# Kernel tuning notes

Measured on AMD Instinct MI355X. Metric: run time of the kernel, lower is better.

Reference implementation:

```python
import jax, jax.numpy as jnp
import numpy as np

N_NODES = 100000
N_EDGES = 6400000
D_IN = 256
OUT = 2        # heads=1, out_channels=2 -> H*C = 2
NEG_SLOPE = 0.2


def setup_inputs() -> dict:
    key = jax.random.key(0)
    ks = jax.random.split(key, 10)
    x = jax.random.normal(ks[0], (N_NODES, D_IN), dtype=jnp.float32)
    edge_index = jax.random.randint(ks[1], (2, N_EDGES), 0, N_NODES, dtype=jnp.int64)
    edge_attr = jax.random.normal(ks[2], (N_EDGES, 1), dtype=jnp.float32)
    s = 1.0 / np.sqrt(D_IN)
    # GATv2Conv params: lin_l (src), lin_r (dst) with bias; lin_edge no bias; att [H*C]; out bias
    Wl = jax.random.normal(ks[3], (D_IN, OUT), dtype=jnp.float32) * s
    bl = jnp.zeros((OUT,), dtype=jnp.float32)
    Wr = jax.random.normal(ks[4], (D_IN, OUT), dtype=jnp.float32) * s
    br = jnp.zeros((OUT,), dtype=jnp.float32)
    We = jax.random.normal(ks[5], (1, OUT), dtype=jnp.float32)
    att = jax.random.normal(ks[6], (OUT,), dtype=jnp.float32)
    bias = jnp.zeros((OUT,), dtype=jnp.float32)
    return {"x": x, "edge_index": edge_index, "edge_attr": edge_attr,
            "Wl": Wl, "bl": bl, "Wr": Wr, "br": br, "We": We,
            "att": att, "bias": bias}


def reference(x, edge_index, edge_attr, Wl, bl, Wr, br, We, att, bias):
    N = x.shape[0]
    src, tgt = edge_index[0], edge_index[1]  # messages flow src -> tgt
    xl = x @ Wl + bl                          # [N, OUT] source-side transform
    xr = x @ Wr + br                          # [N, OUT] target-side transform
    # per-edge GATv2 score: leaky_relu(xl_j + xr_i + W_e e_ij) . att
    m = xl[src] + xr[tgt] + edge_attr @ We    # [E, OUT]
    m = jax.nn.leaky_relu(m, NEG_SLOPE)
    alpha = m @ att                           # [E]
    # segment softmax over edges sharing the same target node
    amax = jax.ops.segment_max(alpha, tgt, num_segments=N)
    amax = jnp.where(jnp.isfinite(amax), amax, 0.0)
    ex = jnp.exp(alpha - amax[tgt])
    denom = jax.ops.segment_sum(ex, tgt, num_segments=N)
    a = ex / (denom[tgt] + 1e-16)             # [E]
    out = jax.ops.segment_sum(a[:, None] * xl[src], tgt, num_segments=N)
    return out + bias
```

## Files before the change

kernel.cpp:

```cpp
#include <hip/hip_runtime.h>

#define N_NODES 100000
#define N_EDGES 6400000
#define D_IN 256
constexpr float NEG_SLOPE = 0.2f;

#define NR 32
#define RANGE 3125
#define NG 16

#define NCH 1280
#define CHE 5000
#define CAP 232
#define HALFCAP 116
#define CPG 80
#define PFLAT (CPG * HALFCAP)
#define NB ((PFLAT + 1023) / 1024)
#define BBLK 256
#define CBLK 1024

#define FCHE 400000


__global__ void node_transform(const float* __restrict__ x,
                               const float* __restrict__ Wl, const float* __restrict__ bl,
                               const float* __restrict__ Wr, const float* __restrict__ br,
                               float* __restrict__ xl, float* __restrict__ xr) {
    int wave = (blockIdx.x * blockDim.x + threadIdx.x) >> 6;
    int lane = threadIdx.x & 63;
    if (wave >= N_NODES) return;
    const float4 xv  = *reinterpret_cast<const float4*>(x + (size_t)wave * D_IN + lane * 4);
    const float4 wlA = *reinterpret_cast<const float4*>(Wl + lane * 8);
    const float4 wlB = *reinterpret_cast<const float4*>(Wl + lane * 8 + 4);
    const float4 wrA = *reinterpret_cast<const float4*>(Wr + lane * 8);
    const float4 wrB = *reinterpret_cast<const float4*>(Wr + lane * 8 + 4);
    float sl0 = xv.x*wlA.x + xv.y*wlA.z + xv.z*wlB.x + xv.w*wlB.z;
    float sl1 = xv.x*wlA.y + xv.y*wlA.w + xv.z*wlB.y + xv.w*wlB.w;
    float sr0 = xv.x*wrA.x + xv.y*wrA.z + xv.z*wrB.x + xv.w*wrB.z;
    float sr1 = xv.x*wrA.y + xv.y*wrA.w + xv.z*wrB.y + xv.w*wrB.w;
    #pragma unroll
    for (int o = 32; o > 0; o >>= 1) {
        sl0 += __shfl_xor(sl0, o);
        sl1 += __shfl_xor(sl1, o);
        sr0 += __shfl_xor(sr0, o);
        sr1 += __shfl_xor(sr1, o);
    }
    if (lane == 0) {
        xl[2*wave]   = sl0 + bl[0];
        xl[2*wave+1] = sl1 + bl[1];
        xr[2*wave]   = sr0 + br[0];
        xr[2*wave+1] = sr1 + br[1];
    }
}

__global__ void detect_dtype(const int* __restrict__ ei32, int* __restrict__ flag) {
    int lane = threadIdx.x;
    int v = ei32[2 * lane + 1];
    unsigned long long nz = __ballot(v != 0);
    if (lane == 0) *flag = (nz == 0ull) ? 1 : 0;
}


__device__ __forceinline__ void bucket_one(int src, int tgt, float ea,
                                           float2* __restrict__ recs,
                                           int* __restrict__ cnt, int c) {
    const int r  = tgt / RANGE;
    const int li = tgt - r * RANGE;
    const int slot = atomicAdd(&cnt[r], 1);
    if (slot < CAP) {
        float2 rec;
        rec.x = __uint_as_float((unsigned)src | ((unsigned)li << 17));
        rec.y = ea;
        recs[(size_t)(c * NR + r) * CAP + slot] = rec;
    }
}

template <bool IS64>
__device__ __forceinline__ void bucket_loop(const void* __restrict__ ei,
                                            const float* __restrict__ eattr,
                                            float2* __restrict__ recs,
                                            int* __restrict__ cnt, int c) {
    const int base = c * CHE;
    const int end  = base + CHE;
    for (int j = 0; j < CHE; j += BBLK * 4) {
        const int e0 = base + j + (int)threadIdx.x * 4;
        if (e0 + 4 <= end) {
            int4 sv, tv;
            if (IS64) {
                const int4* ps = (const int4*)((const long long*)ei + e0);
                int4 a = ps[0], b = ps[1];
                sv = make_int4(a.x, a.z, b.x, b.z);
                const int4* pt = (const int4*)((const long long*)ei + N_EDGES + e0);
                int4 cc = pt[0], dd = pt[1];
                tv = make_int4(cc.x, cc.z, dd.x, dd.z);
            } else {
                sv = *(const int4*)((const int*)ei + e0);
                tv = *(const int4*)((const int*)ei + N_EDGES + e0);
            }
            const float4 ev = *(const float4*)(eattr + e0);
            bucket_one(sv.x, tv.x, ev.x, recs, cnt, c);
            bucket_one(sv.y, tv.y, ev.y, recs, cnt, c);
            bucket_one(sv.z, tv.z, ev.z, recs, cnt, c);
            bucket_one(sv.w, tv.w, ev.w, recs, cnt, c);
        } else if (e0 < end) {
            for (int e = e0; e < end && e < e0 + 4; ++e) {
                int src, tgt;
                if (IS64) { src = (int)((const long long*)ei)[e]; tgt = (int)((const long long*)ei)[N_EDGES + e]; }
                else      { src = ((const int*)ei)[e];            tgt = ((const int*)ei)[N_EDGES + e]; }
                bucket_one(src, tgt, eattr[e], recs, cnt, c);
            }
        }
    }
}

__global__ __launch_bounds__(BBLK) void bucket_pass(const void* __restrict__ ei,
                                                    const float* __restrict__ eattr,
                                                    float2* __restrict__ recs,
                                                    int* __restrict__ counts,
                                                    const int* __restrict__ flag) {
    __shared__ int cnt[NR];
    const int c = blockIdx.x;
    if (threadIdx.x < NR) cnt[threadIdx.x] = 0;
    __syncthreads();
    if (*flag) bucket_loop<true >(ei, eattr, recs, cnt, c);
    else       bucket_loop<false>(ei, eattr, recs, cnt, c);
    __syncthreads();
    if (threadIdx.x < NR) {
        int v = cnt[threadIdx.x];
        counts[c * NR + threadIdx.x] = v < CAP ? v : CAP;
    }
}

__global__ __launch_bounds__(CBLK, 8) void gather_accum(const float2* __restrict__ recs,
                                                        const int* __restrict__ counts,
                                                        const float* __restrict__ xl,
                                                        const float* __restrict__ xr,
                                                        const float* __restrict__ We,
                                                        const float* __restrict__ att,
                                                        float* __restrict__ partial) {
    __shared__ float  acc[RANGE * 3];
    __shared__ float2 xrs[RANGE];
    __shared__ int    tag[RANGE];
    __shared__ int    s_n[CPG];
    const int r = blockIdx.x & (NR - 1);
    const int g = blockIdx.x >> 5;
    const int lo = r * RANGE;
    for (int i = threadIdx.x; i < RANGE * 3; i += CBLK) acc[i] = 0.f;
    for (int i = threadIdx.x; i < RANGE; i += CBLK) xrs[i] = ((const float2*)xr)[lo + i];
    for (int i = threadIdx.x; i < CPG; i += CBLK) s_n[i] = counts[(g * CPG + i) * NR + r];
    __syncthreads();
    const float we0 = We[0], we1 = We[1];
    const float a0 = att[0], a1 = att[1];
    const float2* xl2 = (const float2*)xl;
    const int c0 = g * CPG;
    const int tid = threadIdx.x;

    auto fetch_pair = [&](int pidx, unsigned& vm) -> float4 {
        float4 out = make_float4(0.f, 0.f, 0.f, 0.f);
        vm = 0u;
        if (pidx < PFLAT) {
            const int cc = pidx / HALFCAP;
            const int i  = pidx - cc * HALFCAP;
            const int n  = s_n[cc];
            if (2 * i < n) {
                const float2* seg = recs + (size_t)((c0 + cc) * NR + r) * CAP;
                out = ((const float4*)seg)[i];
                vm = (2 * i + 1 < n) ? 3u : 1u;
            }
        }
        return out;
    };

    unsigned vCur, vNxt, vFly;
    float4 curP = fetch_pair(tid, vCur);
    float4 nxtP = fetch_pair(CBLK + tid, vNxt);
    float2 xsA0 = make_float2(0.f, 0.f), xsA1 = make_float2(0.f, 0.f);
    if (vCur & 1u) xsA0 = xl2[__float_as_uint(curP.x) & 0x1FFFF];
    if (vCur & 2u) xsA1 = xl2[__float_as_uint(curP.z) & 0x1FFFF];

    bool d0 = false, d1 = false;
    int  dl0 = 0, dl1 = 0;
    float dc00 = 0.f, dc01 = 0.f, de0 = 0.f, dc10 = 0.f, dc11 = 0.f, de1 = 0.f;

    for (int b = 0; b < NB; ++b) {
        float4 flyP = fetch_pair((b + 2) * CBLK + tid, vFly);
        float2 xsB0 = make_float2(0.f, 0.f), xsB1 = make_float2(0.f, 0.f);
        if (vNxt & 1u) xsB0 = xl2[__float_as_uint(nxtP.x) & 0x1FFFF];
        if (vNxt & 2u) xsB1 = xl2[__float_as_uint(nxtP.z) & 0x1FFFF];

        const bool h0 = (vCur & 1u) != 0u, h1 = (vCur & 2u) != 0u;
        int li0 = 0, li1 = 0;
        float ex0 = 0.f, cv00 = 0.f, cv01 = 0.f;
        float ex1 = 0.f, cv10 = 0.f, cv11 = 0.f;
        if (h0) {
            const unsigned p = __float_as_uint(curP.x);
            li0 = p >> 17;
            const float2 xt = xrs[li0];
            float m0 = xsA0.x + xt.x + curP.y * we0;
            float m1 = xsA0.y + xt.y + curP.y * we1;
            m0 = m0 > 0.f ? m0 : NEG_SLOPE * m0;
            m1 = m1 > 0.f ? m1 : NEG_SLOPE * m1;
            ex0  = __expf(m0 * a0 + m1 * a1);
            cv00 = ex0 * xsA0.x;
            cv01 = ex0 * xsA0.y;
            tag[li0] = tid;
        }
        if (h1) {
            const unsigned p = __float_as_uint(curP.z);
            li1 = p >> 17;
            const float2 xt = xrs[li1];
            float m0 = xsA1.x + xt.x + curP.w * we0;
            float m1 = xsA1.y + xt.y + curP.w * we1;
            m0 = m0 > 0.f ? m0 : NEG_SLOPE * m0;
            m1 = m1 > 0.f ? m1 : NEG_SLOPE * m1;
            ex1  = __expf(m0 * a0 + m1 * a1);
            cv10 = ex1 * xsA1.x;
            cv11 = ex1 * xsA1.y;
            tag[li1] = tid;
        }
        if (d0) {
            float* bp = acc + dl0 * 3;
            atomicAdd(bp + 0, dc00); atomicAdd(bp + 1, dc01); atomicAdd(bp + 2, de0);
            d0 = false;
        }
        if (d1) {
            float* bp = acc + dl1 * 3;
            atomicAdd(bp + 0, dc10); atomicAdd(bp + 1, dc11); atomicAdd(bp + 2, de1);
            d1 = false;
        }
        __syncthreads();
        if (h0) {
            if (tag[li0] == tid) {
                float* bp = acc + li0 * 3;
                bp[0] += cv00; bp[1] += cv01; bp[2] += ex0;
            } else {
                d0 = true; dl0 = li0; dc00 = cv00; dc01 = cv01; de0 = ex0;
            }
        }
        if (h1) {
            if (tag[li1] == tid) {
                float* bp = acc + li1 * 3;
                bp[0] += cv10; bp[1] += cv11; bp[2] += ex1;
            } else {
                d1 = true; dl1 = li1; dc10 = cv10; dc11 = cv11; de1 = ex1;
            }
        }
        __syncthreads();
        curP = nxtP; vCur = vNxt; xsA0 = xsB0; xsA1 = xsB1;
        nxtP = flyP; vNxt = vFly;
    }
    if (d0) {
        float* bp = acc + dl0 * 3;
        atomicAdd(bp + 0, dc00); atomicAdd(bp + 1, dc01); atomicAdd(bp + 2, de0);
    }
    if (d1) {
        float* bp = acc + dl1 * 3;
        atomicAdd(bp + 0, dc10); atomicAdd(bp + 1, dc11); atomicAdd(bp + 2, de1);
    }
    __syncthreads();

    float* dst = partial + (size_t)(r * NG + g) * (RANGE * 3);
    for (int i = threadIdx.x; i < RANGE * 3; i += CBLK) dst[i] = acc[i];
}

template <bool IS64>
__device__ __forceinline__ void scan_loop(const void* __restrict__ ei,
                                          const float* __restrict__ eattr,
                                          const float2* __restrict__ xl2,
                                          const float2* __restrict__ xr2,
                                          float we0, float we1, float a0, float a1,
                                          int lo, int eBeg, int eEnd,
                                          float* __restrict__ acc) {
    for (int e = eBeg + (int)threadIdx.x; e < eEnd; e += CBLK) {
        int tgt;
        if (IS64) tgt = (int)((const long long*)ei)[N_EDGES + e];
        else      tgt = ((const int*)ei)[N_EDGES + e];
        unsigned li = (unsigned)(tgt - lo);
        if (li < RANGE) {
            int src;
            if (IS64) src = (int)((const long long*)ei)[e];
            else      src = ((const int*)ei)[e];
            const float ea = eattr[e];
            const float2 xs = xl2[src];
            const float2 xt = xr2[tgt];
            float m0 = xs.x + xt.x + ea * we0;
            float m1 = xs.y + xt.y + ea * we1;
            m0 = m0 > 0.f ? m0 : NEG_SLOPE * m0;
            m1 = m1 > 0.f ? m1 : NEG_SLOPE * m1;
            const float ex = __expf(m0 * a0 + m1 * a1);
            float* b = acc + li * 3u;
            atomicAdd(b + 0, ex * xs.x);
            atomicAdd(b + 1, ex * xs.y);
            atomicAdd(b + 2, ex);
        }
    }
}

__global__ __launch_bounds__(CBLK) void edge_scan(const void* __restrict__ ei,
                                                  const float* __restrict__ eattr,
                                                  const float* __restrict__ xl,
                                                  const float* __restrict__ xr,
                                                  const float* __restrict__ We,
                                                  const float* __restrict__ att,
                                                  float* __restrict__ partial,
                                                  const int* __restrict__ flag) {
    __shared__ float acc[RANGE * 3];
    const int r = blockIdx.x & (NR - 1);
    const int g = blockIdx.x >> 5;
    for (int i = threadIdx.x; i < RANGE * 3; i += CBLK) acc[i] = 0.f;
    __syncthreads();
    const int lo = r * RANGE;
    const int eBeg = g * FCHE, eEnd = eBeg + FCHE;
    const float we0 = We[0], we1 = We[1];
    const float a0 = att[0], a1 = att[1];
    if (*flag)
        scan_loop<true >(ei, eattr, (const float2*)xl, (const float2*)xr, we0, we1, a0, a1, lo, eBeg, eEnd, acc);
    else
        scan_loop<false>(ei, eattr, (const float2*)xl, (const float2*)xr, we0, we1, a0, a1, lo, eBeg, eEnd, acc);
    __syncthreads();
    float* dst = partial + (size_t)(r * NG + g) * (RANGE * 3);
    for (int i = threadIdx.x; i < RANGE * 3; i += CBLK) dst[i] = acc[i];
}

__global__ void reduce_partials(const float* __restrict__ partial,
                                const float* __restrict__ bias, float* __restrict__ out) {
    int i = blockIdx.x * blockDim.x + threadIdx.x;
    if (i >= N_NODES) return;
    const int r = i / RANGE;
    const int li = i - r * RANGE;
    float n0 = 0.f, n1 = 0.f, d = 0.f;
    #pragma unroll 4
    for (int g = 0; g < NG; ++g) {
        const float* p = partial + (size_t)(r * NG + g) * (RANGE * 3) + (size_t)li * 3;
        n0 += p[0]; n1 += p[1]; d += p[2];
    }
    d += 1e-16f;
    float2 o;
    o.x = n0 / d + bias[0];
    o.y = n1 / d + bias[1];
    ((float2*)out)[i] = o;
}

__global__ void edge_pass_atomic(const void* __restrict__ ei,
                                 const float* __restrict__ eattr,
                                 const float* __restrict__ xl, const float* __restrict__ xr,
                                 const float* __restrict__ We, const float* __restrict__ att,
                                 float* __restrict__ acc4, const int* __restrict__ flag) {
    const int is64 = *flag;
    const float we0 = We[0], we1 = We[1];
    const float a0 = att[0], a1 = att[1];
    const int stride = gridDim.x * blockDim.x;
    for (int e = blockIdx.x * blockDim.x + threadIdx.x; e < N_EDGES; e += stride) {
        int src, tgt;
        if (is64) { src = (int)((const long long*)ei)[e]; tgt = (int)((const long long*)ei)[N_EDGES + e]; }
        else      { src = ((const int*)ei)[e];            tgt = ((const int*)ei)[N_EDGES + e]; }
        const float ea = eattr[e];
        const float2 xs = ((const float2*)xl)[src];
        const float2 xt = ((const float2*)xr)[tgt];
        float m0 = xs.x + xt.x + ea * we0;
        float m1 = xs.y + xt.y + ea * we1;
        m0 = m0 > 0.f ? m0 : NEG_SLOPE * m0;
        m1 = m1 > 0.f ? m1 : NEG_SLOPE * m1;
        const float ex = __expf(m0 * a0 + m1 * a1);
        float* b = acc4 + (size_t)tgt * 4;
        atomicAdd(b + 0, ex * xs.x);
        atomicAdd(b + 1, ex * xs.y);
        atomicAdd(b + 2, ex);
    }
}

__global__ void finalize4(const float* __restrict__ acc4,
                          const float* __restrict__ bias, float* __restrict__ out) {
    int i = blockIdx.x * blockDim.x + threadIdx.x;
    if (i >= N_NODES) return;
    const float4 a = ((const float4*)acc4)[i];
    const float d = a.z + 1e-16f;
    float2 o;
    o.x = a.x / d + bias[0];
    o.y = a.y / d + bias[1];
    ((float2*)out)[i] = o;
}

extern "C" void kernel_launch(void* const* d_in, const int* in_sizes, int n_in,
                              void* d_out, int out_size, void* d_ws, size_t ws_size,
                              hipStream_t stream) {
    const float* x    = (const float*)d_in[0];
    const void*  ei   = d_in[1];
    const float* ea   = (const float*)d_in[2];
    const float* Wl   = (const float*)d_in[3];
    const float* bl   = (const float*)d_in[4];
    const float* Wr   = (const float*)d_in[5];
    const float* br   = (const float*)d_in[6];
    const float* We   = (const float*)d_in[7];
    const float* att  = (const float*)d_in[8];
    const float* bias = (const float*)d_in[9];

    float* ws      = (float*)d_ws;
    float* xl      = ws;
    float* xr      = ws + 2 * N_NODES;
    float* partial = ws + 4 * N_NODES;
    const size_t partial_floats = (size_t)NR * NG * RANGE * 3;
    float* recs_f  = partial + partial_floats;
    const size_t recs_floats = (size_t)NCH * NR * CAP * 2;
    int*   counts  = (int*)(recs_f + recs_floats);

    const size_t need_bucket = (4 * (size_t)N_NODES + partial_floats + recs_floats
                                + (size_t)NCH * NR + 16) * sizeof(float);
    const size_t need_scan   = (4 * (size_t)N_NODES + partial_floats + 16) * sizeof(float);

    node_transform<<<(N_NODES * 64) / 256, 256, 0, stream>>>(x, Wl, bl, Wr, br, xl, xr);

    if (ws_size >= need_bucket) {
        int* flag = counts + (size_t)NCH * NR;
        detect_dtype<<<1, 64, 0, stream>>>((const int*)ei, flag);
        bucket_pass<<<NCH, BBLK, 0, stream>>>(ei, ea, (float2*)recs_f, counts, flag);
        gather_accum<<<NR * NG, CBLK, 0, stream>>>((const float2*)recs_f, counts,
                                                   xl, xr, We, att, partial);
        reduce_partials<<<(N_NODES + 255) / 256, 256, 0, stream>>>(partial, bias, (float*)d_out);
    } else if (ws_size >= need_scan) {
        int* flag = (int*)(partial + partial_floats);
        detect_dtype<<<1, 64, 0, stream>>>((const int*)ei, flag);
        edge_scan<<<NR * NG, CBLK, 0, stream>>>(ei, ea, xl, xr, We, att, partial, flag);
        reduce_partials<<<(N_NODES + 255) / 256, 256, 0, stream>>>(partial, bias, (float*)d_out);
    } else {
        float* acc4 = ws + 4 * N_NODES;
        int* flag = (int*)(acc4 + 4 * (size_t)N_NODES);
        hipMemsetAsync(acc4, 0, (size_t)N_NODES * 4 * sizeof(float), stream);
        detect_dtype<<<1, 64, 0, stream>>>((const int*)ei, flag);
        edge_pass_atomic<<<4096, 256, 0, stream>>>(ei, ea, xl, xr, We, att, acc4, flag);
        finalize4<<<(N_NODES + 255) / 256, 256, 0, stream>>>(acc4, bias, (float*)d_out);
    }
}
```

Baseline: 124.7 us.

## Fuse node transform, dtype detect and bucketing; coarsen buckets with wave-aggregated slots

Merges the node linear transform, the index dtype detection and the edge bucketing pass into one launch, using separate block ranges for bucketing and node work. Buckets are coarsened from 32 to 16 target ranges, with larger capacity, and slot allocation uses ballot-based wave aggregation so each bucket takes one shared atomic per wave. Each gather block reads its coarse bucket and filters records down to its half range, so every record is read twice. The node transform now packs four nodes per wave. The goal is fewer launches and less shared-atomic contention, at the cost of duplicated record reads and a serial 16-way ballot loop per edge.

```diff
diff --git a/kernel.cpp b/kernel.cpp
--- a/kernel.cpp
+++ b/kernel.cpp
@@ -5,73 +5,55 @@
 #define D_IN 256
 constexpr float NEG_SLOPE = 0.2f;
 
-#define NR 32
+#define NRANGES 32
 #define RANGE 3125
 #define NG 16
 
+#define NRSEG 16
+#define SEGRANGE 6250
 #define NCH 1280
 #define CHE 5000
-#define CAP 232
-#define HALFCAP 116
+#define CAP 416
+#define HALFCAP 208
 #define CPG 80
 #define PFLAT (CPG * HALFCAP)
 #define NB ((PFLAT + 1023) / 1024)
-#define BBLK 256
+#define ABLK 256
 #define CBLK 1024
-
+#define NODE_BLKS 6250
 #define FCHE 400000
 
 
-__global__ void node_transform(const float* __restrict__ x,
-                               const float* __restrict__ Wl, const float* __restrict__ bl,
-                               const float* __restrict__ Wr, const float* __restrict__ br,
-                               float* __restrict__ xl, float* __restrict__ xr) {
-    int wave = (blockIdx.x * blockDim.x + threadIdx.x) >> 6;
-    int lane = threadIdx.x & 63;
-    if (wave >= N_NODES) return;
-    const float4 xv  = *reinterpret_cast<const float4*>(x + (size_t)wave * D_IN + lane * 4);
-    const float4 wlA = *reinterpret_cast<const float4*>(Wl + lane * 8);
-    const float4 wlB = *reinterpret_cast<const float4*>(Wl + lane * 8 + 4);
-    const float4 wrA = *reinterpret_cast<const float4*>(Wr + lane * 8);
-    const float4 wrB = *reinterpret_cast<const float4*>(Wr + lane * 8 + 4);
-    float sl0 = xv.x*wlA.x + xv.y*wlA.z + xv.z*wlB.x + xv.w*wlB.z;
-    float sl1 = xv.x*wlA.y + xv.y*wlA.w + xv.z*wlB.y + xv.w*wlB.w;
-    float sr0 = xv.x*wrA.x + xv.y*wrA.z + xv.z*wrB.x + xv.w*wrB.z;
-    float sr1 = xv.x*wrA.y + xv.y*wrA.w + xv.z*wrB.y + xv.w*wrB.w;
+__device__ __forceinline__ int alloc_slot(int r, int* __restrict__ cnt) {
+    const int lane = threadIdx.x & 63;
+    const unsigned long long lt = (1ull << lane) - 1ull;
+    int slot = 0;
     #pragma unroll
-    for (int o = 32; o > 0; o >>= 1) {
-        sl0 += __shfl_xor(sl0, o);
-        sl1 += __shfl_xor(sl1, o);
-        sr0 += __shfl_xor(sr0, o);
-        sr1 += __shfl_xor(sr1, o);
-    }
-    if (lane == 0) {
-        xl[2*wave]   = sl0 + bl[0];
-        xl[2*wave+1] = sl1 + bl[1];
-        xr[2*wave]   = sr0 + br[0];
-        xr[2*wave+1] = sr1 + br[1];
-    }
-}
-
-__global__ void detect_dtype(const int* __restrict__ ei32, int* __restrict__ flag) {
-    int lane = threadIdx.x;
-    int v = ei32[2 * lane + 1];
-    unsigned long long nz = __ballot(v != 0);
-    if (lane == 0) *flag = (nz == 0ull) ? 1 : 0;
-}
-
+    for (int rr = 0; rr < NRSEG; ++rr) {
+        const unsigned long long m = __ballot(r == rr);
+        if (r == rr) {
+            const int before = __popcll(m & lt);
+            const int leader = __ffsll((unsigned long long)m) - 1;
+            int base = 0;
+            if (lane == leader) base = atomicAdd(&cnt[rr], __popcll(m));
+            base = __shfl(base, leader);
+            slot = base + before;
+        }
+    }
+    return slot;
+}
 
 __device__ __forceinline__ void bucket_one(int src, int tgt, float ea,
                                            float2* __restrict__ recs,
                                            int* __restrict__ cnt, int c) {
-    const int r  = tgt / RANGE;
-    const int li = tgt - r * RANGE;
-    const int slot = atomicAdd(&cnt[r], 1);
+    const int r  = tgt / SEGRANGE;
+    const int li = tgt - r * SEGRANGE;
+    const int slot = alloc_slot(r, cnt);
     if (slot < CAP) {
         float2 rec;
         rec.x = __uint_as_float((unsigned)src | ((unsigned)li << 17));
         rec.y = ea;
-        recs[(size_t)(c * NR + r) * CAP + slot] = rec;
+        recs[(size_t)(c * NRSEG + r) * CAP + slot] = rec;
     }
 }
 
@@ -82,7 +64,7 @@
                                             int* __restrict__ cnt, int c) {
     const int base = c * CHE;
     const int end  = base + CHE;
-    for (int j = 0; j < CHE; j += BBLK * 4) {
+    for (int j = 0; j < CHE; j += ABLK * 4) {
         const int e0 = base + j + (int)threadIdx.x * 4;
         if (e0 + 4 <= end) {
             int4 sv, tv;
@@ -113,41 +95,93 @@
     }
 }
 
-__global__ __launch_bounds__(BBLK) void bucket_pass(const void* __restrict__ ei,
-                                                    const float* __restrict__ eattr,
-                                                    float2* __restrict__ recs,
-                                                    int* __restrict__ counts,
-                                                    const int* __restrict__ flag) {
-    __shared__ int cnt[NR];
-    const int c = blockIdx.x;
-    if (threadIdx.x < NR) cnt[threadIdx.x] = 0;
-    __syncthreads();
-    if (*flag) bucket_loop<true >(ei, eattr, recs, cnt, c);
-    else       bucket_loop<false>(ei, eattr, recs, cnt, c);
-    __syncthreads();
-    if (threadIdx.x < NR) {
-        int v = cnt[threadIdx.x];
-        counts[c * NR + threadIdx.x] = v < CAP ? v : CAP;
-    }
-}
-
-__global__ __launch_bounds__(CBLK, 8) void gather_accum(const float2* __restrict__ recs,
-                                                        const int* __restrict__ counts,
-                                                        const float* __restrict__ xl,
-                                                        const float* __restrict__ xr,
-                                                        const float* __restrict__ We,
-                                                        const float* __restrict__ att,
-                                                        float* __restrict__ partial) {
+__device__ __forceinline__ void node_body(const float* __restrict__ x,
+                                          const float* __restrict__ Wl, const float* __restrict__ bl,
+                                          const float* __restrict__ Wr, const float* __restrict__ br,
+                                          float* __restrict__ xl, float* __restrict__ xr, int bid) {
+    const int w    = bid * 4 + ((int)threadIdx.x >> 6);
+    const int lane = threadIdx.x & 63;
+    const int sub  = lane >> 4;
+    const int l16  = lane & 15;
+    const int n    = w * 4 + sub;
+    float sl0 = 0.f, sl1 = 0.f, sr0 = 0.f, sr1 = 0.f;
+    #pragma unroll
+    for (int q = 0; q < 4; ++q) {
+        const int k = q * 64 + l16 * 4;
+        const float4 xv  = *(const float4*)(x + (size_t)n * D_IN + k);
+        const float4 wlA = *(const float4*)(Wl + 2 * k);
+        const float4 wlB = *(const float4*)(Wl + 2 * k + 4);
+        const float4 wrA = *(const float4*)(Wr + 2 * k);
+        const float4 wrB = *(const float4*)(Wr + 2 * k + 4);
+        sl0 += xv.x*wlA.x + xv.y*wlA.z + xv.z*wlB.x + xv.w*wlB.z;
+        sl1 += xv.x*wlA.y + xv.y*wlA.w + xv.z*wlB.y + xv.w*wlB.w;
+        sr0 += xv.x*wrA.x + xv.y*wrA.z + xv.z*wrB.x + xv.w*wrB.z;
+        sr1 += xv.x*wrA.y + xv.y*wrA.w + xv.z*wrB.y + xv.w*wrB.w;
+    }
+    #pragma unroll
+    for (int o = 8; o > 0; o >>= 1) {
+        sl0 += __shfl_xor(sl0, o);
+        sl1 += __shfl_xor(sl1, o);
+        sr0 += __shfl_xor(sr0, o);
+        sr1 += __shfl_xor(sr1, o);
+    }
+    if (l16 == 0) {
+        xl[2*n]   = sl0 + bl[0];
+        xl[2*n+1] = sl1 + bl[1];
+        xr[2*n]   = sr0 + br[0];
+        xr[2*n+1] = sr1 + br[1];
+    }
+}
+
+__global__ __launch_bounds__(ABLK) void fused_node_bucket(
+        const float* __restrict__ x,
+        const float* __restrict__ Wl, const float* __restrict__ bl,
+        const float* __restrict__ Wr, const float* __restrict__ br,
+        const void* __restrict__ ei, const float* __restrict__ eattr,
+        float* __restrict__ xl, float* __restrict__ xr,
+        float2* __restrict__ recs, int* __restrict__ counts) {
+    if (blockIdx.x < NCH) {
+        __shared__ int cnt[NRSEG];
+        __shared__ int sflag;
+        const int c = blockIdx.x;
+        if (threadIdx.x < NRSEG) cnt[threadIdx.x] = 0;
+        if (threadIdx.x < 64) {
+            int v = ((const int*)ei)[2 * threadIdx.x + 1];
+            unsigned long long nz = __ballot(v != 0);
+            if (threadIdx.x == 0) sflag = (nz == 0ull) ? 1 : 0;
+        }
+        __syncthreads();
+        if (sflag) bucket_loop<true >(ei, eattr, recs, cnt, c);
+        else       bucket_loop<false>(ei, eattr, recs, cnt, c);
+        __syncthreads();
+        if (threadIdx.x < NRSEG) {
+            int v = cnt[threadIdx.x];
+            counts[c * NRSEG + threadIdx.x] = v < CAP ? v : CAP;
+        }
+    } else {
+        node_body(x, Wl, bl, Wr, br, xl, xr, (int)blockIdx.x - NCH);
+    }
+}
+
+__global__ __launch_bounds__(CBLK, 8) void gather_accum(
+        const float2* __restrict__ recs, const int* __restrict__ counts,
+        const float* __restrict__ xl, const float* __restrict__ xr,
+        const float* __restrict__ We, const float* __restrict__ att,
+        float* __restrict__ partial) {
     __shared__ float  acc[RANGE * 3];
     __shared__ float2 xrs[RANGE];
     __shared__ int    tag[RANGE];
     __shared__ int    s_n[CPG];
-    const int r = blockIdx.x & (NR - 1);
-    const int g = blockIdx.x >> 5;
-    const int lo = r * RANGE;
+    const int b      = blockIdx.x;
+    const int r16    = b & 15;
+    const int h      = (b >> 4) & 1;
+    const int g      = b >> 5;
+    const int rr     = r16 * 2 + h;
+    const int lo     = rr * RANGE;
+    const int liBase = h * RANGE;
     for (int i = threadIdx.x; i < RANGE * 3; i += CBLK) acc[i] = 0.f;
     for (int i = threadIdx.x; i < RANGE; i += CBLK) xrs[i] = ((const float2*)xr)[lo + i];
-    for (int i = threadIdx.x; i < CPG; i += CBLK) s_n[i] = counts[(g * CPG + i) * NR + r];
+    for (int i = threadIdx.x; i < CPG; i += CBLK) s_n[i] = counts[(g * CPG + i) * NRSEG + r16];
     __syncthreads();
     const float we0 = We[0], we1 = We[1];
     const float a0 = att[0], a1 = att[1];
@@ -163,9 +197,13 @@
             const int i  = pidx - cc * HALFCAP;
             const int n  = s_n[cc];
             if (2 * i < n) {
-                const float2* seg = recs + (size_t)((c0 + cc) * NR + r) * CAP;
+                const float2* seg = recs + (size_t)((c0 + cc) * NRSEG + r16) * CAP;
                 out = ((const float4*)seg)[i];
-                vm = (2 * i + 1 < n) ? 3u : 1u;
+                unsigned v = 0u;
+                if ((unsigned)((int)(__float_as_uint(out.x) >> 17) - liBase) < RANGE) v |= 1u;
+                if ((2 * i + 1 < n) &&
+                    (unsigned)((int)(__float_as_uint(out.z) >> 17) - liBase) < RANGE) v |= 2u;
+                vm = v;
             }
         }
         return out;
@@ -182,8 +220,8 @@
     int  dl0 = 0, dl1 = 0;
     float dc00 = 0.f, dc01 = 0.f, de0 = 0.f, dc10 = 0.f, dc11 = 0.f, de1 = 0.f;
 
-    for (int b = 0; b < NB; ++b) {
-        float4 flyP = fetch_pair((b + 2) * CBLK + tid, vFly);
+    for (int bi = 0; bi < NB; ++bi) {
+        float4 flyP = fetch_pair((bi + 2) * CBLK + tid, vFly);
         float2 xsB0 = make_float2(0.f, 0.f), xsB1 = make_float2(0.f, 0.f);
         if (vNxt & 1u) xsB0 = xl2[__float_as_uint(nxtP.x) & 0x1FFFF];
         if (vNxt & 2u) xsB1 = xl2[__float_as_uint(nxtP.z) & 0x1FFFF];
@@ -193,8 +231,7 @@
         float ex0 = 0.f, cv00 = 0.f, cv01 = 0.f;
         float ex1 = 0.f, cv10 = 0.f, cv11 = 0.f;
         if (h0) {
-            const unsigned p = __float_as_uint(curP.x);
-            li0 = p >> 17;
+            li0 = (int)(__float_as_uint(curP.x) >> 17) - liBase;
             const float2 xt = xrs[li0];
             float m0 = xsA0.x + xt.x + curP.y * we0;
             float m1 = xsA0.y + xt.y + curP.y * we1;
@@ -206,8 +243,7 @@
             tag[li0] = tid;
         }
         if (h1) {
-            const unsigned p = __float_as_uint(curP.z);
-            li1 = p >> 17;
+            li1 = (int)(__float_as_uint(curP.z) >> 17) - liBase;
             const float2 xt = xrs[li1];
             float m0 = xsA1.x + xt.x + curP.w * we0;
             float m1 = xsA1.y + xt.y + curP.w * we1;
@@ -233,17 +269,13 @@
             if (tag[li0] == tid) {
                 float* bp = acc + li0 * 3;
                 bp[0] += cv00; bp[1] += cv01; bp[2] += ex0;
-            } else {
-                d0 = true; dl0 = li0; dc00 = cv00; dc01 = cv01; de0 = ex0;
-            }
+            } else { d0 = true; dl0 = li0; dc00 = cv00; dc01 = cv01; de0 = ex0; }
         }
         if (h1) {
             if (tag[li1] == tid) {
                 float* bp = acc + li1 * 3;
                 bp[0] += cv10; bp[1] += cv11; bp[2] += ex1;
-            } else {
-                d1 = true; dl1 = li1; dc10 = cv10; dc11 = cv11; de1 = ex1;
-            }
+            } else { d1 = true; dl1 = li1; dc10 = cv10; dc11 = cv11; de1 = ex1; }
         }
         __syncthreads();
         curP = nxtP; vCur = vNxt; xsA0 = xsB0; xsA1 = xsB1;
@@ -259,8 +291,41 @@
     }
     __syncthreads();
 
-    float* dst = partial + (size_t)(r * NG + g) * (RANGE * 3);
+    float* dst = partial + (size_t)(rr * NG + g) * (RANGE * 3);
     for (int i = threadIdx.x; i < RANGE * 3; i += CBLK) dst[i] = acc[i];
+}
+
+__global__ void reduce_partials(const float* __restrict__ partial,
+                                const float* __restrict__ bias, float* __restrict__ out) {
+    int i = blockIdx.x * blockDim.x + threadIdx.x;
+    if (i >= N_NODES) return;
+    const int r = i / RANGE;
+    const int li = i - r * RANGE;
+    float n0 = 0.f, n1 = 0.f, d = 0.f;
+    #pragma unroll 4
+    for (int g = 0; g < NG; ++g) {
+        const float* p = partial + (size_t)(r * NG + g) * (RANGE * 3) + (size_t)li * 3;
+        n0 += p[0]; n1 += p[1]; d += p[2];
+    }
+    d += 1e-16f;
+    float2 o;
+    o.x = n0 / d + bias[0];
+    o.y = n1 / d + bias[1];
+    ((float2*)out)[i] = o;
+}
+
+__global__ __launch_bounds__(ABLK) void node_only(const float* __restrict__ x,
+                                                  const float* __restrict__ Wl, const float* __restrict__ bl,
+                                                  const float* __restrict__ Wr, const float* __restrict__ br,
+                                                  float* __restrict__ xl, float* __restrict__ xr) {
+    node_body(x, Wl, bl, Wr, br, xl, xr, (int)blockIdx.x);
+}
+
+__global__ void detect_dtype(const int* __restrict__ ei32, int* __restrict__ flag) {
+    int lane = threadIdx.x;
+    int v = ei32[2 * lane + 1];
+    unsigned long long nz = __ballot(v != 0);
+    if (lane == 0) *flag = (nz == 0ull) ? 1 : 0;
 }
 
 template <bool IS64>
@@ -305,7 +370,7 @@
                                                   float* __restrict__ partial,
                                                   const int* __restrict__ flag) {
     __shared__ float acc[RANGE * 3];
-    const int r = blockIdx.x & (NR - 1);
+    const int r = blockIdx.x & (NRANGES - 1);
     const int g = blockIdx.x >> 5;
     for (int i = threadIdx.x; i < RANGE * 3; i += CBLK) acc[i] = 0.f;
     __syncthreads();
@@ -320,25 +385,6 @@
     __syncthreads();
     float* dst = partial + (size_t)(r * NG + g) * (RANGE * 3);
     for (int i = threadIdx.x; i < RANGE * 3; i += CBLK) dst[i] = acc[i];
-}
-
-__global__ void reduce_partials(const float* __restrict__ partial,
-                                const float* __restrict__ bias, float* __restrict__ out) {
-    int i = blockIdx.x * blockDim.x + threadIdx.x;
-    if (i >= N_NODES) return;
-    const int r = i / RANGE;
-    const int li = i - r * RANGE;
-    float n0 = 0.f, n1 = 0.f, d = 0.f;
-    #pragma unroll 4
-    for (int g = 0; g < NG; ++g) {
-        const float* p = partial + (size_t)(r * NG + g) * (RANGE * 3) + (size_t)li * 3;
-        n0 += p[0]; n1 += p[1]; d += p[2];
-    }
-    d += 1e-16f;
-    float2 o;
-    o.x = n0 / d + bias[0];
-    o.y = n1 / d + bias[1];
-    ((float2*)out)[i] = o;
 }
 
 __global__ void edge_pass_atomic(const void* __restrict__ ei,
@@ -399,35 +445,35 @@
     float* xl      = ws;
     float* xr      = ws + 2 * N_NODES;
     float* partial = ws + 4 * N_NODES;
-    const size_t partial_floats = (size_t)NR * NG * RANGE * 3;
+    const size_t partial_floats = (size_t)NRANGES * NG * RANGE * 3;
     float* recs_f  = partial + partial_floats;
-    const size_t recs_floats = (size_t)NCH * NR * CAP * 2;
+    const size_t recs_floats = (size_t)NCH * NRSEG * CAP * 2;
     int*   counts  = (int*)(recs_f + recs_floats);
+    int*   flag    = counts + (size_t)NCH * NRSEG;
 
     const size_t need_bucket = (4 * (size_t)N_NODES + partial_floats + recs_floats
-                                + (size_t)NCH * NR + 16) * sizeof(float);
+                                + (size_t)NCH * NRSEG + 16) * sizeof(float);
     const size_t need_scan   = (4 * (size_t)N_NODES + partial_floats + 16) * sizeof(float);
 
-    node_transform<<<(N_NODES * 64) / 256, 256, 0, stream>>>(x, Wl, bl, Wr, br, xl, xr);
-
     if (ws_size >= need_bucket) {
-        int* flag = counts + (size_t)NCH * NR;
-        detect_dtype<<<1, 64, 0, stream>>>((const int*)ei, flag);
-        bucket_pass<<<NCH, BBLK, 0, stream>>>(ei, ea, (float2*)recs_f, counts, flag);
-        gather_accum<<<NR * NG, CBLK, 0, stream>>>((const float2*)recs_f, counts,
-                                                   xl, xr, We, att, partial);
+        fused_node_bucket<<<NCH + NODE_BLKS, ABLK, 0, stream>>>(
+            x, Wl, bl, Wr, br, ei, ea, xl, xr, (float2*)recs_f, counts);
+        gather_accum<<<NRANGES * NG, CBLK, 0, stream>>>(
+            (const float2*)recs_f, counts, xl, xr, We, att, partial);
         reduce_partials<<<(N_NODES + 255) / 256, 256, 0, stream>>>(partial, bias, (float*)d_out);
     } else if (ws_size >= need_scan) {
-        int* flag = (int*)(partial + partial_floats);
-        detect_dtype<<<1, 64, 0, stream>>>((const int*)ei, flag);
-        edge_scan<<<NR * NG, CBLK, 0, stream>>>(ei, ea, xl, xr, We, att, partial, flag);
+        int* f2 = (int*)(partial + partial_floats);
+        node_only<<<NODE_BLKS, ABLK, 0, stream>>>(x, Wl, bl, Wr, br, xl, xr);
+        detect_dtype<<<1, 64, 0, stream>>>((const int*)ei, f2);
+        edge_scan<<<NRANGES * NG, CBLK, 0, stream>>>(ei, ea, xl, xr, We, att, partial, f2);
         reduce_partials<<<(N_NODES + 255) / 256, 256, 0, stream>>>(partial, bias, (float*)d_out);
     } else {
         float* acc4 = ws + 4 * N_NODES;
-        int* flag = (int*)(acc4 + 4 * (size_t)N_NODES);
+        int* f3 = (int*)(acc4 + 4 * (size_t)N_NODES);
         hipMemsetAsync(acc4, 0, (size_t)N_NODES * 4 * sizeof(float), stream);
-        detect_dtype<<<1, 64, 0, stream>>>((const int*)ei, flag);
-        edge_pass_atomic<<<4096, 256, 0, stream>>>(ei, ea, xl, xr, We, att, acc4, flag);
+        node_only<<<NODE_BLKS, ABLK, 0, stream>>>(x, Wl, bl, Wr, br, xl, xr);
+        detect_dtype<<<1, 64, 0, stream>>>((const int*)ei, f3);
+        edge_pass_atomic<<<4096, 256, 0, stream>>>(ei, ea, xl, xr, We, att, acc4, f3);
         finalize4<<<(N_NODES + 255) / 256, 256, 0, stream>>>(acc4, bias, (float*)d_out);
     }
 }
```

Result: slower. 131.8 us (+5.7%).
